# Kernel tuning notes

Hardware: AMD Instinct MI355X
Metric: run time of the kernel (lower is better)

Reference implementation:

```python
import jax, jax.numpy as jnp
import numpy as np

PAD = 1  # symmetric spatial padding (pad_H == pad_W enforced by the module)


def setup_inputs() -> dict:
    key = jax.random.key(0)
    k1, k2, k3 = jax.random.split(key, 3)
    N, C, F, H, W, HH, WW = 32, 128, 128, 32, 32, 3, 3
    x = jax.random.normal(k1, (N, C, H, W), dtype=jnp.float32)
    weight = jax.random.normal(k2, (F, C, HH, WW), dtype=jnp.float32) * 0.05
    bias = jax.random.normal(k3, (F,), dtype=jnp.float32) * 0.05
    return {"x": x, "weight": weight, "bias": bias}


def reference(x, weight, bias):
    # Conv2dfft forward, no compression (compress_rate=0, preserve_energy=100,
    # next_power2=False, stride=1, real_fft path).
    N, C, H, W = x.shape
    F, _, HH, WW = weight.shape
    pad = PAD
    out_H = H - HH + 1 + 2 * pad
    out_W = W - WW + 1 + 2 * pad
    HHH = max(out_H, HH)
    WWW = max(out_W, WW)
    init_H = H + 2 * pad + HHH - 1  # full linear-conv FFT size
    init_W = W + 2 * pad + WWW - 1
    # torch_pad(input, (pad_W, pad_W + fft_pad_W, pad_H, pad_H + fft_pad_H))
    xp = jnp.pad(x, ((0, 0), (0, 0), (pad, init_H - pad - H), (pad, init_W - pad - W)))
    # torch_pad(filter, (0, fft_pad_W, 0, fft_pad_H))
    wp = jnp.pad(weight, ((0, 0), (0, 0), (0, init_H - HH), (0, init_W - WW)))
    xf = jnp.fft.rfft2(xp)          # [N, C, init_H, init_W//2+1] complex
    wf = jnp.fft.rfft2(wp)          # [F, C, init_H, init_W//2+1] complex
    # Cross-correlation in frequency domain: xfft * conj(yfft), contracted
    # over input channels C per frequency bin. This is exactly the math of the
    # module's fast_multiply (3-real-mult complex product via matmul) applied
    # to the conjugated filter spectrum.
    of = jnp.einsum('nchw,fchw->nfhw', xf, jnp.conj(wf))
    out = jnp.fft.irfft2(of, s=(init_H, init_W))[..., :out_H, :out_W]
    return out + bias[None, :, None, None]
```

## Files before the change

kernel.cpp:

```cpp
#include <hip/hip_runtime.h>


typedef short bf16x8 __attribute__((ext_vector_type(8)));
typedef short bf16x4 __attribute__((ext_vector_type(4)));
typedef float f32x4  __attribute__((ext_vector_type(4)));

__device__ __forceinline__ short f2bf(float f) {
  unsigned u = __builtin_bit_cast(unsigned, f);
  u = (u + 0x7fffu + ((u >> 16) & 1u)) >> 16;
  return (short)u;
}

__global__ __launch_bounds__(256) void conv_wprep(const float* __restrict__ w,
                                                  short* __restrict__ bc2) {
  int tid  = blockIdx.x * 256 + threadIdx.x;
  int j    = tid & 7;
  int l15  = (tid >> 3) & 15;
  int quad = (tid >> 7) & 3;
  int fblk = (tid >> 9) & 7;
  int g2   = tid >> 12;
  int chunk = g2 / 9, tap = g2 % 9;
  int p = tap / 3, q = tap % 3;
  int f = fblk * 16 + l15;
  int c = chunk * 32 + quad * 8 + j;
  bc2[tid] = f2bf(w[(f * 128 + c) * 9 + p * 3 + q]);
}

__global__ __launch_bounds__(256, 1) void conv_main(
    const float* __restrict__ x, const short* __restrict__ bc2,
    const float* __restrict__ bias, float* __restrict__ out) {
  __shared__ __align__(16) short xs[2][6 * 34 * 36];

  const int t    = threadIdx.x;
  const int lane = t & 63;
  const int wv   = t >> 6;
  const int n_img = blockIdx.x >> 3;
  const int h0    = (blockIdx.x & 7) << 2;

  const int l15  = lane & 15;
  const int quad = lane >> 4;
  const int f_off  = (wv & 1) * 64;
  const int s_rowb = (wv >> 1) * 2;

  const int w_ = t & 31;
  const int g  = t >> 5;
  const float* xb = x + n_img * 128 * 1024;

  if (t < 192) {
    int buf = t / 96, rem = t % 96;
    int r = rem / 16, rem2 = rem % 16;
    int colsel = rem2 / 8, q4 = rem2 % 8;
    *(int2*)&xs[buf][(r * 34 + colsel * 33) * 36 + q4 * 4] = make_int2(0, 0);
  }

  f32x4 acc[4][4] = {};
  float xv[24];

#pragma unroll
  for (int r = 0; r < 6; ++r) {
    int hr = h0 - 1 + r;
    bool ok = (unsigned)hr < 32u;
#pragma unroll
    for (int cc = 0; cc < 4; ++cc)
      xv[r * 4 + cc] = ok ? xb[((g * 4 + cc) * 32 + hr) * 32 + w_] : 0.f;
  }
#pragma unroll
  for (int r = 0; r < 6; ++r) {
    bf16x4 v = { f2bf(xv[r*4+0]), f2bf(xv[r*4+1]), f2bf(xv[r*4+2]), f2bf(xv[r*4+3]) };
    *(bf16x4*)&xs[0][(r * 34 + w_ + 1) * 36 + g * 4] = v;
  }
  __syncthreads();

#pragma unroll
  for (int chunk = 0; chunk < 4; ++chunk) {
    if (chunk < 3) {
#pragma unroll
      for (int r = 0; r < 6; ++r) {
        int hr = h0 - 1 + r;
        bool ok = (unsigned)hr < 32u;
#pragma unroll
        for (int cc = 0; cc < 4; ++cc)
          xv[r * 4 + cc] =
              ok ? xb[(((chunk + 1) * 32 + g * 4 + cc) * 32 + hr) * 32 + w_] : 0.f;
      }
    }
    const short* xbuf = xs[chunk & 1];
#pragma unroll
    for (int p = 0; p < 3; ++p) {
#pragma unroll
      for (int q = 0; q < 3; ++q) {
        const int tap = p * 3 + q;
        const short* wb = bc2 + ((chunk * 9 + tap) * 8 + (wv & 1) * 4) * 512;
        bf16x8 af[4], bfr[4];
#pragma unroll
        for (int mt = 0; mt < 4; ++mt)
          af[mt] = *(const bf16x8*)&wb[mt * 512 + lane * 8];
#pragma unroll
        for (int nt = 0; nt < 4; ++nt) {
          int r   = s_rowb + (nt >> 1) + p;
          int col = (nt & 1) * 16 + l15 + q;
          bfr[nt] = *(const bf16x8*)&xbuf[(r * 34 + col) * 36 + quad * 8];
        }
#pragma unroll
        for (int mt = 0; mt < 4; ++mt)
#pragma unroll
          for (int nt = 0; nt < 4; ++nt)
            acc[mt][nt] = __builtin_amdgcn_mfma_f32_16x16x32_bf16(
                af[mt], bfr[nt], acc[mt][nt], 0, 0, 0);
      }
    }
    if (chunk < 3) {
#pragma unroll
      for (int r = 0; r < 6; ++r) {
        bf16x4 v = { f2bf(xv[r*4+0]), f2bf(xv[r*4+1]), f2bf(xv[r*4+2]), f2bf(xv[r*4+3]) };
        *(bf16x4*)&xs[(chunk + 1) & 1][(r * 34 + w_ + 1) * 36 + g * 4] = v;
      }
      __syncthreads();
    }
  }

#pragma unroll
  for (int nt = 0; nt < 4; ++nt) {
    int h = h0 + s_rowb + (nt >> 1);
    int w_out = (nt & 1) * 16 + l15;
#pragma unroll
    for (int mt = 0; mt < 4; ++mt) {
#pragma unroll
      for (int reg = 0; reg < 4; ++reg) {
        int f = f_off + mt * 16 + quad * 4 + reg;
        out[((n_img * 128 + f) * 32 + h) * 32 + w_out] = acc[mt][nt][reg] + bias[f];
      }
    }
  }
}

extern "C" void kernel_launch(void* const* d_in, const int* in_sizes, int n_in,
                              void* d_out, int out_size, void* d_ws, size_t ws_size,
                              hipStream_t stream) {
  const float* x    = (const float*)d_in[0];
  const float* w    = (const float*)d_in[1];
  const float* bias = (const float*)d_in[2];
  float* out = (float*)d_out;
  short* bc2 = (short*)d_ws;

  conv_wprep<<<576, 256, 0, stream>>>(w, bc2);
  conv_main<<<256, 256, 0, stream>>>(x, bc2, bias, out);
}
```

Before: 95.41 us.

## Prefetch filter fragments one tap-row ahead and pad LDS row stride

The main kernel now double-buffers the A-operand (filter) fragments in registers, loading the next row of three taps (12 bf16x8 vectors) from global memory while the current row's MFMAs execute, instead of loading them right before use. The LDS row stride is changed from 36 to 40 shorts, presumably to change the bank mapping of the B-fragment reads. The weight-prep kernel now reads the weights coalesced and scatters its writes. The extra 96 VGPRs of prefetch buffers raise register pressure, though the kernel already runs with one block per CU.

```diff
diff --git a/kernel.cpp b/kernel.cpp
--- a/kernel.cpp
+++ b/kernel.cpp
@@ -13,23 +13,32 @@
 
 __global__ __launch_bounds__(256) void conv_wprep(const float* __restrict__ w,
                                                   short* __restrict__ bc2) {
-  int tid  = blockIdx.x * 256 + threadIdx.x;
-  int j    = tid & 7;
-  int l15  = (tid >> 3) & 15;
-  int quad = (tid >> 7) & 3;
-  int fblk = (tid >> 9) & 7;
-  int g2   = tid >> 12;
-  int chunk = g2 / 9, tap = g2 % 9;
-  int p = tap / 3, q = tap % 3;
-  int f = fblk * 16 + l15;
-  int c = chunk * 32 + quad * 8 + j;
-  bc2[tid] = f2bf(w[(f * 128 + c) * 9 + p * 3 + q]);
+  int tid = blockIdx.x * 256 + threadIdx.x;
+  float v = w[tid];
+  int f   = tid / 1152;
+  int rem = tid - f * 1152;
+  int c   = rem / 9;
+  int tap = rem - c * 9;
+  int dst = ((((c >> 5) * 9 + tap) * 8 + (f >> 4)) * 512)
+          + (((c >> 3) & 3) * 16 + (f & 15)) * 8
+          + (c & 7);
+  bc2[dst] = f2bf(v);
+}
+
+__device__ __forceinline__ void load_af(bf16x8* dst, const short* __restrict__ bc2,
+                                        int chunk, int p, int fsel, int lane) {
+  const short* base = bc2 + (((chunk * 9 + p * 3) * 8 + fsel * 4) * 512) + lane * 8;
+#pragma unroll
+  for (int q = 0; q < 3; ++q)
+#pragma unroll
+    for (int mt = 0; mt < 4; ++mt)
+      dst[q * 4 + mt] = *(const bf16x8*)(base + (q * 8 + mt) * 512);
 }
 
 __global__ __launch_bounds__(256, 1) void conv_main(
     const float* __restrict__ x, const short* __restrict__ bc2,
     const float* __restrict__ bias, float* __restrict__ out) {
-  __shared__ __align__(16) short xs[2][6 * 34 * 36];
+  __shared__ __align__(16) short xs[2][6 * 34 * 40];
 
   const int t    = threadIdx.x;
   const int lane = t & 63;
@@ -39,18 +48,22 @@
 
   const int l15  = lane & 15;
   const int quad = lane >> 4;
-  const int f_off  = (wv & 1) * 64;
+  const int fsel   = wv & 1;
+  const int f_off  = fsel * 64;
   const int s_rowb = (wv >> 1) * 2;
 
   const int w_ = t & 31;
   const int g  = t >> 5;
   const float* xb = x + n_img * 128 * 1024;
 
+  bf16x8 afA[12], afB[12];
+  load_af(afA, bc2, 0, 0, fsel, lane);
+
   if (t < 192) {
     int buf = t / 96, rem = t % 96;
     int r = rem / 16, rem2 = rem % 16;
     int colsel = rem2 / 8, q4 = rem2 % 8;
-    *(int2*)&xs[buf][(r * 34 + colsel * 33) * 36 + q4 * 4] = make_int2(0, 0);
+    *(int2*)&xs[buf][(r * 34 + colsel * 33) * 40 + q4 * 4] = make_int2(0, 0);
   }
 
   f32x4 acc[4][4] = {};
@@ -67,7 +80,7 @@
 #pragma unroll
   for (int r = 0; r < 6; ++r) {
     bf16x4 v = { f2bf(xv[r*4+0]), f2bf(xv[r*4+1]), f2bf(xv[r*4+2]), f2bf(xv[r*4+3]) };
-    *(bf16x4*)&xs[0][(r * 34 + w_ + 1) * 36 + g * 4] = v;
+    *(bf16x4*)&xs[0][(r * 34 + w_ + 1) * 40 + g * 4] = v;
   }
   __syncthreads();
 
@@ -87,33 +100,33 @@
     const short* xbuf = xs[chunk & 1];
 #pragma unroll
     for (int p = 0; p < 3; ++p) {
+      const int grp = chunk * 3 + p;
+      const bf16x8* cur = (grp & 1) ? afB : afA;
+      bf16x8*       nxt = (grp & 1) ? afA : afB;
+      if (grp < 11)
+        load_af(nxt, bc2, (grp + 1) / 3, (grp + 1) % 3, fsel, lane);
 #pragma unroll
       for (int q = 0; q < 3; ++q) {
-        const int tap = p * 3 + q;
-        const short* wb = bc2 + ((chunk * 9 + tap) * 8 + (wv & 1) * 4) * 512;
-        bf16x8 af[4], bfr[4];
-#pragma unroll
-        for (int mt = 0; mt < 4; ++mt)
-          af[mt] = *(const bf16x8*)&wb[mt * 512 + lane * 8];
+        bf16x8 bfr[4];
 #pragma unroll
         for (int nt = 0; nt < 4; ++nt) {
           int r   = s_rowb + (nt >> 1) + p;
           int col = (nt & 1) * 16 + l15 + q;
-          bfr[nt] = *(const bf16x8*)&xbuf[(r * 34 + col) * 36 + quad * 8];
+          bfr[nt] = *(const bf16x8*)&xbuf[(r * 34 + col) * 40 + quad * 8];
         }
 #pragma unroll
         for (int mt = 0; mt < 4; ++mt)
 #pragma unroll
           for (int nt = 0; nt < 4; ++nt)
             acc[mt][nt] = __builtin_amdgcn_mfma_f32_16x16x32_bf16(
-                af[mt], bfr[nt], acc[mt][nt], 0, 0, 0);
+                cur[q * 4 + mt], bfr[nt], acc[mt][nt], 0, 0, 0);
       }
     }
     if (chunk < 3) {
 #pragma unroll
       for (int r = 0; r < 6; ++r) {
         bf16x4 v = { f2bf(xv[r*4+0]), f2bf(xv[r*4+1]), f2bf(xv[r*4+2]), f2bf(xv[r*4+3]) };
-        *(bf16x4*)&xs[(chunk + 1) & 1][(r * 34 + w_ + 1) * 36 + g * 4] = v;
+        *(bf16x4*)&xs[(chunk + 1) & 1][(r * 34 + w_ + 1) * 40 + g * 4] = v;
       }
       __syncthreads();
     }
```

Result: faster. 87.48 us (-8.3%).
